# Optimization experiments

Measured on AMD Instinct MI355X. Metric: run time of the kernel, lower is better.

The kernel has to match this reference:

```python
import jax, jax.numpy as jnp
import numpy as np

HIDDEN = 4096
NUM_EXPERTS = 64
TOPK = 2
N_TOKENS = 16384


def setup_inputs() -> dict:
    key = jax.random.key(0)
    k_x, k_w, k_b = jax.random.split(key, 3)
    x = jax.random.normal(k_x, (N_TOKENS, HIDDEN), dtype=jnp.float32)
    # torch.nn.Linear: weight [out, in], bias [out], uniform(-1/sqrt(in), 1/sqrt(in))
    bound = 1.0 / np.sqrt(HIDDEN)
    W = jax.random.uniform(k_w, (NUM_EXPERTS, HIDDEN), dtype=jnp.float32, minval=-bound, maxval=bound)
    b = jax.random.uniform(k_b, (NUM_EXPERTS,), dtype=jnp.float32, minval=-bound, maxval=bound)
    return {"x": x, "W": W, "b": b}


def reference(x, W, b):
    # logits: [N, E] = x @ W.T + b
    logits = jnp.einsum("nh,eh->ne", x, W) + b
    probs = jax.nn.softmax(logits, axis=1)
    # torch.topk along dim=1 returns (values, indices), sorted descending
    values, indices = jax.lax.top_k(probs, TOPK)
    return values, indices
```

## Files before the change

### kernel.cpp

```cpp
#include <hip/hip_runtime.h>
#include <hip/hip_bf16.h>
#include <math.h>

#define HIDDEN   4096
#define NEXP     64
#define NTOK     16384
#define KCHUNKS  8
#define KC       (HIDDEN / KCHUNKS)
#define BK       32
#define BT       64
#define LDSS     68

__global__ __launch_bounds__(64, 2)
void gemm_partial(const float* __restrict__ x, const float* __restrict__ W,
                  float* __restrict__ part) {
    __shared__ float Xs[BK][LDSS];
    __shared__ float Ws[BK][LDSS];

    const int tid  = threadIdx.x;
    const int tile = blockIdx.x;
    const int kc   = blockIdx.y;
    const int t0   = tile * BT;

    const int lrow = tid & 7;
    const int lcol = tid >> 3;
    const int i    = tid & 7;
    const int j    = tid >> 3;

    float acc[8][8];
#pragma unroll
    for (int m = 0; m < 8; ++m)
#pragma unroll
        for (int e = 0; e < 8; ++e) acc[m][e] = 0.f;

    for (int kb = 0; kb < KC / BK; ++kb) {
        const int kg = kc * KC + kb * BK + lrow * 4;
#pragma unroll
        for (int p = 0; p < 8; ++p) {
            const int r = p * 8 + lcol;
            const float4 xv = *(const float4*)&x[(size_t)(t0 + r) * HIDDEN + kg];
            Xs[lrow * 4 + 0][r] = xv.x;
            Xs[lrow * 4 + 1][r] = xv.y;
            Xs[lrow * 4 + 2][r] = xv.z;
            Xs[lrow * 4 + 3][r] = xv.w;
            const float4 wv = *(const float4*)&W[(size_t)r * HIDDEN + kg];
            Ws[lrow * 4 + 0][r] = wv.x;
            Ws[lrow * 4 + 1][r] = wv.y;
            Ws[lrow * 4 + 2][r] = wv.z;
            Ws[lrow * 4 + 3][r] = wv.w;
        }
        __syncthreads();
#pragma unroll
        for (int kk = 0; kk < BK; ++kk) {
            const float4 xa = *(const float4*)&Xs[kk][i * 8];
            const float4 xb = *(const float4*)&Xs[kk][i * 8 + 4];
            const float4 wa = *(const float4*)&Ws[kk][j * 8];
            const float4 wb = *(const float4*)&Ws[kk][j * 8 + 4];
            const float xr[8] = {xa.x, xa.y, xa.z, xa.w, xb.x, xb.y, xb.z, xb.w};
            const float wr[8] = {wa.x, wa.y, wa.z, wa.w, wb.x, wb.y, wb.z, wb.w};
#pragma unroll
            for (int m = 0; m < 8; ++m)
#pragma unroll
                for (int e = 0; e < 8; ++e)
                    acc[m][e] = fmaf(xr[m], wr[e], acc[m][e]);
        }
        __syncthreads();
    }

    float* dst = part + ((size_t)kc * NTOK + t0) * NEXP;
#pragma unroll
    for (int m = 0; m < 8; ++m) {
        const int tok = i * 8 + m;
#pragma unroll
        for (int h = 0; h < 2; ++h) {
            float4 o = make_float4(acc[m][h * 4 + 0], acc[m][h * 4 + 1],
                                   acc[m][h * 4 + 2], acc[m][h * 4 + 3]);
            *(float4*)&dst[(size_t)tok * NEXP + j * 8 + h * 4] = o;
        }
    }
}

__global__ __launch_bounds__(256)
void softmax_top2(const float* __restrict__ part, const float* __restrict__ bias,
                  float* __restrict__ out) {
    const int lane = threadIdx.x & 63;
    const int wid  = threadIdx.x >> 6;
    const int t    = blockIdx.x * 4 + wid;

    float l = bias[lane];
#pragma unroll
    for (int c = 0; c < KCHUNKS; ++c)
        l += part[((size_t)c * NTOK + t) * NEXP + lane];

    float m = l;
#pragma unroll
    for (int s = 32; s > 0; s >>= 1)
        m = fmaxf(m, __shfl_xor(m, s, 64));

    float ssum = expf(l - m);
#pragma unroll
    for (int s = 32; s > 0; s >>= 1)
        ssum += __shfl_xor(ssum, s, 64);

    float v1 = l; int i1 = lane;
#pragma unroll
    for (int s = 32; s > 0; s >>= 1) {
        float ov = __shfl_xor(v1, s, 64);
        int   oi = __shfl_xor(i1, s, 64);
        if (ov > v1 || (ov == v1 && oi < i1)) { v1 = ov; i1 = oi; }
    }
    float v2 = (lane == i1) ? -INFINITY : l;
    int   i2 = lane;
#pragma unroll
    for (int s = 32; s > 0; s >>= 1) {
        float ov = __shfl_xor(v2, s, 64);
        int   oi = __shfl_xor(i2, s, 64);
        if (ov > v2 || (ov == v2 && oi < i2)) { v2 = ov; i2 = oi; }
    }

    if (lane == 0) {
        const float inv = 1.0f / ssum;
        out[(size_t)t * 2 + 0] = inv;
        out[(size_t)t * 2 + 1] = expf(v2 - m) * inv;
        out[(size_t)2 * NTOK + t * 2 + 0] = (float)i1;
        out[(size_t)2 * NTOK + t * 2 + 1] = (float)i2;
    }
}

extern "C" void kernel_launch(void* const* d_in, const int* in_sizes, int n_in,
                              void* d_out, int out_size, void* d_ws, size_t ws_size,
                              hipStream_t stream) {
    const float* x  = (const float*)d_in[0];
    const float* W  = (const float*)d_in[1];
    const float* b  = (const float*)d_in[2];
    float* out  = (float*)d_out;
    float* part = (float*)d_ws;

    dim3 g1(NTOK / BT, KCHUNKS);
    gemm_partial<<<g1, 64, 0, stream>>>(x, W, part);
    softmax_top2<<<NTOK / 4, 256, 0, stream>>>(part, b, out);
}
```

Baseline: 401.2 us.

## Fuse gating GEMM and softmax-top2 into one kernel with in-block split-K reduction

Replaces the two-kernel design (split-K GEMM writing partials to workspace, then a softmax/top-2 kernel) with one kernel. Each 512-thread block handles 32 tokens, and each of its 8 waves covers a separate K slice. Waves load x and W straight from global memory into registers with no LDS staging, and the partial sums are reduced through LDS before the softmax and top-2 run in the same block. This removes the workspace round trip and the second launch. In exchange, W rows are read strided per lane with no LDS sharing, which relies on cache for reuse and may raise global-load traffic and latency.

```diff
diff --git a/kernel.cpp b/kernel.cpp
--- a/kernel.cpp
+++ b/kernel.cpp
@@ -1,142 +1,121 @@
 #include <hip/hip_runtime.h>
-#include <hip/hip_bf16.h>
 #include <math.h>
 
-#define HIDDEN   4096
-#define NEXP     64
-#define NTOK     16384
-#define KCHUNKS  8
-#define KC       (HIDDEN / KCHUNKS)
-#define BK       32
-#define BT       64
-#define LDSS     68
+#define HIDDEN 4096
+#define NEXP   64
+#define NTOK   16384
+#define BT     32
+#define NW     8
+#define KC     (HIDDEN / NW)
 
-__global__ __launch_bounds__(64, 2)
-void gemm_partial(const float* __restrict__ x, const float* __restrict__ W,
-                  float* __restrict__ part) {
-    __shared__ float Xs[BK][LDSS];
-    __shared__ float Ws[BK][LDSS];
+__global__ __launch_bounds__(512, 4)
+void gating_fused(const float* __restrict__ x, const float* __restrict__ W,
+                  const float* __restrict__ bias, float* __restrict__ out) {
+    __shared__ float red[NW][BT][NEXP];
 
     const int tid  = threadIdx.x;
-    const int tile = blockIdx.x;
-    const int kc   = blockIdx.y;
-    const int t0   = tile * BT;
+    const int lane = tid & 63;
+    const int wid  = tid >> 6;
+    const int t0   = blockIdx.x * BT;
 
-    const int lrow = tid & 7;
-    const int lcol = tid >> 3;
-    const int i    = tid & 7;
-    const int j    = tid >> 3;
+    const int i  = lane & 7;
+    const int j  = lane >> 3;
+    const int k0 = wid * KC;
 
-    float acc[8][8];
+    const float4* xp[4];
+    const float4* wp[8];
 #pragma unroll
-    for (int m = 0; m < 8; ++m)
+    for (int m = 0; m < 4; ++m)
+        xp[m] = (const float4*)&x[(size_t)(t0 + i * 4 + m) * HIDDEN + k0];
+#pragma unroll
+    for (int e = 0; e < 8; ++e)
+        wp[e] = (const float4*)&W[(size_t)(j * 8 + e) * HIDDEN + k0];
+
+    float acc[4][8];
+#pragma unroll
+    for (int m = 0; m < 4; ++m)
 #pragma unroll
         for (int e = 0; e < 8; ++e) acc[m][e] = 0.f;
 
-    for (int kb = 0; kb < KC / BK; ++kb) {
-        const int kg = kc * KC + kb * BK + lrow * 4;
+#pragma unroll 2
+    for (int g = 0; g < KC / 4; ++g) {
+        float4 xv[4], wv[8];
 #pragma unroll
-        for (int p = 0; p < 8; ++p) {
-            const int r = p * 8 + lcol;
-            const float4 xv = *(const float4*)&x[(size_t)(t0 + r) * HIDDEN + kg];
-            Xs[lrow * 4 + 0][r] = xv.x;
-            Xs[lrow * 4 + 1][r] = xv.y;
-            Xs[lrow * 4 + 2][r] = xv.z;
-            Xs[lrow * 4 + 3][r] = xv.w;
-            const float4 wv = *(const float4*)&W[(size_t)r * HIDDEN + kg];
-            Ws[lrow * 4 + 0][r] = wv.x;
-            Ws[lrow * 4 + 1][r] = wv.y;
-            Ws[lrow * 4 + 2][r] = wv.z;
-            Ws[lrow * 4 + 3][r] = wv.w;
-        }
-        __syncthreads();
+        for (int m = 0; m < 4; ++m) xv[m] = xp[m][g];
 #pragma unroll
-        for (int kk = 0; kk < BK; ++kk) {
-            const float4 xa = *(const float4*)&Xs[kk][i * 8];
-            const float4 xb = *(const float4*)&Xs[kk][i * 8 + 4];
-            const float4 wa = *(const float4*)&Ws[kk][j * 8];
-            const float4 wb = *(const float4*)&Ws[kk][j * 8 + 4];
-            const float xr[8] = {xa.x, xa.y, xa.z, xa.w, xb.x, xb.y, xb.z, xb.w};
-            const float wr[8] = {wa.x, wa.y, wa.z, wa.w, wb.x, wb.y, wb.z, wb.w};
+        for (int e = 0; e < 8; ++e) wv[e] = wp[e][g];
+        const float* xf = (const float*)xv;
+        const float* wf = (const float*)wv;
 #pragma unroll
-            for (int m = 0; m < 8; ++m)
+        for (int dk = 0; dk < 4; ++dk)
+#pragma unroll
+            for (int m = 0; m < 4; ++m)
 #pragma unroll
                 for (int e = 0; e < 8; ++e)
-                    acc[m][e] = fmaf(xr[m], wr[e], acc[m][e]);
-        }
-        __syncthreads();
+                    acc[m][e] = fmaf(xf[m * 4 + dk], wf[e * 4 + dk], acc[m][e]);
     }
 
-    float* dst = part + ((size_t)kc * NTOK + t0) * NEXP;
 #pragma unroll
-    for (int m = 0; m < 8; ++m) {
-        const int tok = i * 8 + m;
+    for (int m = 0; m < 4; ++m)
 #pragma unroll
-        for (int h = 0; h < 2; ++h) {
-            float4 o = make_float4(acc[m][h * 4 + 0], acc[m][h * 4 + 1],
-                                   acc[m][h * 4 + 2], acc[m][h * 4 + 3]);
-            *(float4*)&dst[(size_t)tok * NEXP + j * 8 + h * 4] = o;
+        for (int e = 0; e < 8; ++e)
+            red[wid][i * 4 + m][j * 8 + e] = acc[m][e];
+    __syncthreads();
+
+#pragma unroll
+    for (int q = 0; q < 4; ++q) {
+        const int tt = wid * 4 + q;
+
+        float l = bias[lane];
+#pragma unroll
+        for (int c = 0; c < NW; ++c)
+            l += red[c][tt][lane];
+
+        float mx = l;
+#pragma unroll
+        for (int s = 32; s > 0; s >>= 1)
+            mx = fmaxf(mx, __shfl_xor(mx, s, 64));
+
+        float ssum = expf(l - mx);
+#pragma unroll
+        for (int s = 32; s > 0; s >>= 1)
+            ssum += __shfl_xor(ssum, s, 64);
+
+        float v1 = l; int i1 = lane;
+#pragma unroll
+        for (int s = 32; s > 0; s >>= 1) {
+            float ov = __shfl_xor(v1, s, 64);
+            int   oi = __shfl_xor(i1, s, 64);
+            if (ov > v1 || (ov == v1 && oi < i1)) { v1 = ov; i1 = oi; }
         }
-    }
-}
+        float v2 = (lane == i1) ? -INFINITY : l;
+        int   i2 = lane;
+#pragma unroll
+        for (int s = 32; s > 0; s >>= 1) {
+            float ov = __shfl_xor(v2, s, 64);
+            int   oi = __shfl_xor(i2, s, 64);
+            if (ov > v2 || (ov == v2 && oi < i2)) { v2 = ov; i2 = oi; }
+        }
 
-__global__ __launch_bounds__(256)
-void softmax_top2(const float* __restrict__ part, const float* __restrict__ bias,
-                  float* __restrict__ out) {
-    const int lane = threadIdx.x & 63;
-    const int wid  = threadIdx.x >> 6;
-    const int t    = blockIdx.x * 4 + wid;
-
-    float l = bias[lane];
-#pragma unroll
-    for (int c = 0; c < KCHUNKS; ++c)
-        l += part[((size_t)c * NTOK + t) * NEXP + lane];
-
-    float m = l;
-#pragma unroll
-    for (int s = 32; s > 0; s >>= 1)
-        m = fmaxf(m, __shfl_xor(m, s, 64));
-
-    float ssum = expf(l - m);
-#pragma unroll
-    for (int s = 32; s > 0; s >>= 1)
-        ssum += __shfl_xor(ssum, s, 64);
-
-    float v1 = l; int i1 = lane;
-#pragma unroll
-    for (int s = 32; s > 0; s >>= 1) {
-        float ov = __shfl_xor(v1, s, 64);
-        int   oi = __shfl_xor(i1, s, 64);
-        if (ov > v1 || (ov == v1 && oi < i1)) { v1 = ov; i1 = oi; }
-    }
-    float v2 = (lane == i1) ? -INFINITY : l;
-    int   i2 = lane;
-#pragma unroll
-    for (int s = 32; s > 0; s >>= 1) {
-        float ov = __shfl_xor(v2, s, 64);
-        int   oi = __shfl_xor(i2, s, 64);
-        if (ov > v2 || (ov == v2 && oi < i2)) { v2 = ov; i2 = oi; }
-    }
-
-    if (lane == 0) {
-        const float inv = 1.0f / ssum;
-        out[(size_t)t * 2 + 0] = inv;
-        out[(size_t)t * 2 + 1] = expf(v2 - m) * inv;
-        out[(size_t)2 * NTOK + t * 2 + 0] = (float)i1;
-        out[(size_t)2 * NTOK + t * 2 + 1] = (float)i2;
+        if (lane == 0) {
+            const int t = t0 + tt;
+            const float inv = 1.0f / ssum;
+            out[(size_t)t * 2 + 0] = inv;
+            out[(size_t)t * 2 + 1] = expf(v2 - mx) * inv;
+            out[(size_t)2 * NTOK + t * 2 + 0] = (float)i1;
+            out[(size_t)2 * NTOK + t * 2 + 1] = (float)i2;
+        }
     }
 }
 
 extern "C" void kernel_launch(void* const* d_in, const int* in_sizes, int n_in,
                               void* d_out, int out_size, void* d_ws, size_t ws_size,
                               hipStream_t stream) {
-    const float* x  = (const float*)d_in[0];
-    const float* W  = (const float*)d_in[1];
-    const float* b  = (const float*)d_in[2];
-    float* out  = (float*)d_out;
-    float* part = (float*)d_ws;
+    const float* x = (const float*)d_in[0];
+    const float* W = (const float*)d_in[1];
+    const float* b = (const float*)d_in[2];
+    float* out = (float*)d_out;
+    (void)d_ws; (void)ws_size;
 
-    dim3 g1(NTOK / BT, KCHUNKS);
-    gemm_partial<<<g1, 64, 0, stream>>>(x, W, part);
-    softmax_top2<<<NTOK / 4, 256, 0, stream>>>(part, b, out);
+    gating_fused<<<dim3(NTOK / BT), 512, 0, stream>>>(x, W, b, out);
 }
```

Result: slower. 672.3 us (+67.6%).

## Double-buffer GEMM tiles via direct global-to-LDS async loads with swizzled layout

Applied to the files above, without the earlier changes.

Replaces the register-staged, transposed LDS fill with `__builtin_amdgcn_global_load_lds` 16-byte async copies into a double-buffered LDS tile. K-step drops to 16, and an XOR swizzle on the k offset is meant to avoid bank conflicts in the row-major tile. The next tile's copy is issued right after the current tile's fragments are read, so global loads overlap the FMA loop. Block-level barriers are removed because the block is a single wave. This relies on the compiler inserting the right vmcnt waits for the LDS DMA, and on gfx950 supporting 16-byte LDS-direct loads.

```diff
diff --git a/kernel.cpp b/kernel.cpp
--- a/kernel.cpp
+++ b/kernel.cpp
@@ -1,5 +1,4 @@
 #include <hip/hip_runtime.h>
-#include <hip/hip_bf16.h>
 #include <math.h>
 
 #define HIDDEN   4096
@@ -7,25 +6,46 @@
 #define NTOK     16384
 #define KCHUNKS  8
 #define KC       (HIDDEN / KCHUNKS)
-#define BK       32
+#define BK       16
+#define ITERS    (KC / BK)
 #define BT       64
-#define LDSS     68
 
 __global__ __launch_bounds__(64, 2)
 void gemm_partial(const float* __restrict__ x, const float* __restrict__ W,
                   float* __restrict__ part) {
-    __shared__ float Xs[BK][LDSS];
-    __shared__ float Ws[BK][LDSS];
+    __shared__ float lds[2][2][64 * BK];
 
-    const int tid  = threadIdx.x;
+    const int lane = threadIdx.x;
     const int tile = blockIdx.x;
     const int kc   = blockIdx.y;
     const int t0   = tile * BT;
+    const int i    = lane & 7;
+    const int j    = lane >> 3;
+    const int kbase = kc * KC;
 
-    const int lrow = tid & 7;
-    const int lcol = tid >> 3;
-    const int i    = tid & 7;
-    const int j    = tid >> 3;
+    const float* xsrc[4];
+    const float* wsrc[4];
+#pragma unroll
+    for (int p = 0; p < 4; ++p) {
+        const int row = p * 16 + (lane >> 2);
+        const int kk  = 4 * ((lane & 3) ^ ((2 * p + (lane >> 5)) & 3));
+        xsrc[p] = &x[(size_t)(t0 + row) * HIDDEN + kbase + kk];
+        wsrc[p] = &W[(size_t)row * HIDDEN + kbase + kk];
+    }
+
+#define STAGE(buf, itn) do {                                                        \
+    _Pragma("unroll")                                                               \
+    for (int p = 0; p < 4; ++p) {                                                   \
+        __builtin_amdgcn_global_load_lds(                                           \
+            (const __attribute__((address_space(1))) uint32_t*)(xsrc[p] + (itn) * BK), \
+            (__attribute__((address_space(3))) uint32_t*)&lds[buf][0][p * 256],     \
+            16, 0, 0);                                                              \
+        __builtin_amdgcn_global_load_lds(                                           \
+            (const __attribute__((address_space(1))) uint32_t*)(wsrc[p] + (itn) * BK), \
+            (__attribute__((address_space(3))) uint32_t*)&lds[buf][1][p * 256],     \
+            16, 0, 0);                                                              \
+    }                                                                               \
+} while (0)
 
     float acc[8][8];
 #pragma unroll
@@ -33,39 +53,34 @@
 #pragma unroll
         for (int e = 0; e < 8; ++e) acc[m][e] = 0.f;
 
-    for (int kb = 0; kb < KC / BK; ++kb) {
-        const int kg = kc * KC + kb * BK + lrow * 4;
+    STAGE(0, 0);
+
+#pragma unroll 2
+    for (int it = 0; it < ITERS; ++it) {
+        const int cb = it & 1;
+        const int nb = cb ^ 1;
 #pragma unroll
-        for (int p = 0; p < 8; ++p) {
-            const int r = p * 8 + lcol;
-            const float4 xv = *(const float4*)&x[(size_t)(t0 + r) * HIDDEN + kg];
-            Xs[lrow * 4 + 0][r] = xv.x;
-            Xs[lrow * 4 + 1][r] = xv.y;
-            Xs[lrow * 4 + 2][r] = xv.z;
-            Xs[lrow * 4 + 3][r] = xv.w;
-            const float4 wv = *(const float4*)&W[(size_t)r * HIDDEN + kg];
-            Ws[lrow * 4 + 0][r] = wv.x;
-            Ws[lrow * 4 + 1][r] = wv.y;
-            Ws[lrow * 4 + 2][r] = wv.z;
-            Ws[lrow * 4 + 3][r] = wv.w;
-        }
-        __syncthreads();
-#pragma unroll
-        for (int kk = 0; kk < BK; ++kk) {
-            const float4 xa = *(const float4*)&Xs[kk][i * 8];
-            const float4 xb = *(const float4*)&Xs[kk][i * 8 + 4];
-            const float4 wa = *(const float4*)&Ws[kk][j * 8];
-            const float4 wb = *(const float4*)&Ws[kk][j * 8 + 4];
-            const float xr[8] = {xa.x, xa.y, xa.z, xa.w, xb.x, xb.y, xb.z, xb.w};
-            const float wr[8] = {wa.x, wa.y, wa.z, wa.w, wb.x, wb.y, wb.z, wb.w};
+        for (int g = 0; g < 4; ++g) {
+            float4 xv[8], wv[8];
 #pragma unroll
             for (int m = 0; m < 8; ++m)
+                xv[m] = *(const float4*)&lds[cb][0][(i * 8 + m) * BK + ((g * 4) ^ ((i & 3) << 2))];
 #pragma unroll
-                for (int e = 0; e < 8; ++e)
-                    acc[m][e] = fmaf(xr[m], wr[e], acc[m][e]);
+            for (int e = 0; e < 8; ++e)
+                wv[e] = *(const float4*)&lds[cb][1][(j * 8 + e) * BK + ((g * 4) ^ ((j & 3) << 2))];
+            if (g == 0 && it + 1 < ITERS) STAGE(nb, it + 1);
+#pragma unroll
+            for (int dk = 0; dk < 4; ++dk)
+#pragma unroll
+                for (int m = 0; m < 8; ++m) {
+                    const float xs = ((const float*)&xv[m])[dk];
+#pragma unroll
+                    for (int e = 0; e < 8; ++e)
+                        acc[m][e] = fmaf(xs, ((const float*)&wv[e])[dk], acc[m][e]);
+                }
         }
-        __syncthreads();
     }
+#undef STAGE
 
     float* dst = part + ((size_t)kc * NTOK + t0) * NEXP;
 #pragma unroll
```

After: 707.9 us. +76.4%, slower.

## Replace LDS-tiled GEMM with per-lane expert dot products over interleaved W

Applied to the files above, without the earlier changes.

A new pre-pass kernel rewrites W into a K-group-major interleaved layout, so each of the 64 lanes, one per expert, can load its float4 slice with one coalesced access. The GEMM drops shared-memory tiling and barriers. Each wave handles 16 tokens and reads x as broadcast float4 loads, so all lanes read the same address. This removes LDS traffic and syncs and raises occupancy, but register-level reuse is much lower (16 FMAs per x load instead of an 8x8 tile). Throughput then depends heavily on the cache serving the broadcast x loads and repeated W reads.

```diff
diff --git a/kernel.cpp b/kernel.cpp
--- a/kernel.cpp
+++ b/kernel.cpp
@@ -1,5 +1,4 @@
 #include <hip/hip_runtime.h>
-#include <hip/hip_bf16.h>
 #include <math.h>
 
 #define HIDDEN   4096
@@ -7,77 +6,50 @@
 #define NTOK     16384
 #define KCHUNKS  8
 #define KC       (HIDDEN / KCHUNKS)
-#define BK       32
-#define BT       64
-#define LDSS     68
+#define NG       (HIDDEN / 4)
+#define GPC      (KC / 4)
+#define TT       16
 
-__global__ __launch_bounds__(64, 2)
-void gemm_partial(const float* __restrict__ x, const float* __restrict__ W,
+__global__ void winter(const float* __restrict__ W, float* __restrict__ Wti) {
+    const int gid = blockIdx.x * 256 + threadIdx.x;
+    const int e   = gid >> 10;
+    const int g   = gid & 1023;
+    const float4 v = *(const float4*)&W[(size_t)e * HIDDEN + g * 4];
+    *(float4*)&Wti[(size_t)g * 256 + e * 4] = v;
+}
+
+__global__ __launch_bounds__(64, 8)
+void gemm_partial(const float* __restrict__ x, const float* __restrict__ Wti,
                   float* __restrict__ part) {
-    __shared__ float Xs[BK][LDSS];
-    __shared__ float Ws[BK][LDSS];
+    const int lane  = threadIdx.x;
+    const int t0    = blockIdx.x * TT;
+    const int kc    = blockIdx.y;
+    const int gbase = kc * GPC;
 
-    const int tid  = threadIdx.x;
-    const int tile = blockIdx.x;
-    const int kc   = blockIdx.y;
-    const int t0   = tile * BT;
+    float acc[TT];
+#pragma unroll
+    for (int t = 0; t < TT; ++t) acc[t] = 0.f;
 
-    const int lrow = tid & 7;
-    const int lcol = tid >> 3;
-    const int i    = tid & 7;
-    const int j    = tid >> 3;
+    const float* __restrict__ wp = Wti + (size_t)gbase * 256 + lane * 4;
 
-    float acc[8][8];
+#pragma unroll 1
+    for (int g = 0; g < GPC; ++g) {
+        const float4 wq = *(const float4*)(wp + (size_t)g * 256);
 #pragma unroll
-    for (int m = 0; m < 8; ++m)
-#pragma unroll
-        for (int e = 0; e < 8; ++e) acc[m][e] = 0.f;
-
-    for (int kb = 0; kb < KC / BK; ++kb) {
-        const int kg = kc * KC + kb * BK + lrow * 4;
-#pragma unroll
-        for (int p = 0; p < 8; ++p) {
-            const int r = p * 8 + lcol;
-            const float4 xv = *(const float4*)&x[(size_t)(t0 + r) * HIDDEN + kg];
-            Xs[lrow * 4 + 0][r] = xv.x;
-            Xs[lrow * 4 + 1][r] = xv.y;
-            Xs[lrow * 4 + 2][r] = xv.z;
-            Xs[lrow * 4 + 3][r] = xv.w;
-            const float4 wv = *(const float4*)&W[(size_t)r * HIDDEN + kg];
-            Ws[lrow * 4 + 0][r] = wv.x;
-            Ws[lrow * 4 + 1][r] = wv.y;
-            Ws[lrow * 4 + 2][r] = wv.z;
-            Ws[lrow * 4 + 3][r] = wv.w;
+        for (int t = 0; t < TT; ++t) {
+            const float4 xs = *(const float4*)&x[(size_t)(t0 + t) * HIDDEN
+                                                 + kc * KC + g * 4];
+            float a = fmaf(xs.x, wq.x, acc[t]);
+            a       = fmaf(xs.y, wq.y, a);
+            a       = fmaf(xs.z, wq.z, a);
+            acc[t]  = fmaf(xs.w, wq.w, a);
         }
-        __syncthreads();
-#pragma unroll
-        for (int kk = 0; kk < BK; ++kk) {
-            const float4 xa = *(const float4*)&Xs[kk][i * 8];
-            const float4 xb = *(const float4*)&Xs[kk][i * 8 + 4];
-            const float4 wa = *(const float4*)&Ws[kk][j * 8];
-            const float4 wb = *(const float4*)&Ws[kk][j * 8 + 4];
-            const float xr[8] = {xa.x, xa.y, xa.z, xa.w, xb.x, xb.y, xb.z, xb.w};
-            const float wr[8] = {wa.x, wa.y, wa.z, wa.w, wb.x, wb.y, wb.z, wb.w};
-#pragma unroll
-            for (int m = 0; m < 8; ++m)
-#pragma unroll
-                for (int e = 0; e < 8; ++e)
-                    acc[m][e] = fmaf(xr[m], wr[e], acc[m][e]);
-        }
-        __syncthreads();
     }
 
-    float* dst = part + ((size_t)kc * NTOK + t0) * NEXP;
+    float* dst = part + ((size_t)kc * NTOK + t0) * NEXP + lane;
 #pragma unroll
-    for (int m = 0; m < 8; ++m) {
-        const int tok = i * 8 + m;
-#pragma unroll
-        for (int h = 0; h < 2; ++h) {
-            float4 o = make_float4(acc[m][h * 4 + 0], acc[m][h * 4 + 1],
-                                   acc[m][h * 4 + 2], acc[m][h * 4 + 3]);
-            *(float4*)&dst[(size_t)tok * NEXP + j * 8 + h * 4] = o;
-        }
-    }
+    for (int t = 0; t < TT; ++t)
+        dst[(size_t)t * NEXP] = acc[t];
 }
 
 __global__ __launch_bounds__(256)
@@ -135,8 +107,10 @@
     const float* b  = (const float*)d_in[2];
     float* out  = (float*)d_out;
     float* part = (float*)d_ws;
+    float* Wti  = part + (size_t)KCHUNKS * NTOK * NEXP;
 
-    dim3 g1(NTOK / BT, KCHUNKS);
-    gemm_partial<<<g1, 64, 0, stream>>>(x, W, part);
+    winter<<<dim3(256), 256, 0, stream>>>(W, Wti);
+    dim3 g1(NTOK / TT, KCHUNKS);
+    gemm_partial<<<g1, 64, 0, stream>>>(x, Wti, part);
     softmax_top2<<<NTOK / 4, 256, 0, stream>>>(part, b, out);
 }
```

Result: slower. 1.082 ms (+169.8%).
